# Optimization experiments

Hardware: AMD Instinct MI355X
Metric: run time of the kernel (lower is better)

## Reference

```python
import jax, jax.numpy as jnp
import numpy as np

B, T, D, H = 2, 2048, 1024, 16
NEG = -65504.0


def setup_inputs() -> dict:
    key = jax.random.key(0)
    ks = jax.random.split(key, 12)
    std = float(np.sqrt(2.0 / (D + D)))  # xavier_normal for square weights
    inp = {
        'q': jax.random.normal(ks[0], (B, T, D), jnp.float32),
        'k': jax.random.normal(ks[1], (B, T, D), jnp.float32),
        'v': jax.random.normal(ks[2], (B, T, D), jnp.float32),
        'mask': jax.random.randint(ks[3], (B, T), 0, 2, jnp.int32),
        # weights stored as (in, out) so y = x @ W + b
        'Wq': jax.random.normal(ks[4], (D, D), jnp.float32) * std,
        'bq': jnp.zeros((D,), jnp.float32),
        'Wk': jax.random.normal(ks[5], (D, D), jnp.float32) * std,
        'bk': jnp.zeros((D,), jnp.float32),
        'Wv': jax.random.normal(ks[6], (D, D), jnp.float32) * std,
        'bv': jnp.zeros((D,), jnp.float32),
        'Wo': jax.random.normal(ks[7], (D, D), jnp.float32) * std,
        'bo': jnp.zeros((D,), jnp.float32),
    }
    return inp


def reference(q, k, v, mask, Wq, bq, Wk, bk, Wv, bv, Wo, bo):
    b, t, _ = q.shape
    dim_a = Wq.shape[1]
    dh = dim_a // H
    # projections, then split into heads: (b, t, H, dh)
    qh = (q @ Wq + bq).reshape(b, t, H, dh)
    kh = (k @ Wk + bk).reshape(b, t, H, dh)
    vh = (v @ Wv + bv).reshape(b, t, H, dh)
    # NOTE: module scales by 1/sqrt(dim_a) with the FULL dim_a, not per-head
    a = jnp.einsum('bthd,bshd->bhts', qh, kh) / jnp.sqrt(jnp.float32(dim_a))
    # 2D mask broadcasts over query positions: (b, 1, 1, t_keys)
    a = jnp.where(mask[:, None, None, :] == 0, NEG, a)
    a = jax.nn.softmax(a, axis=-1)  # dropout_prob=0 (eval mode)
    o = jnp.einsum('bhts,bshd->bthd', a, vh).reshape(b, t, dim_a)
    return o @ Wo + bo
```

## Files before the change

### kernel.cpp

```cpp
#include <hip/hip_runtime.h>
#include <hip/hip_bf16.h>
#include <math.h>

#define B_ 2
#define T_ 2048
#define D_ 1024
#define H_ 16
#define QSCALE (0.03125f * 1.44269504088896f)

typedef _Float16 f16;
using f16x4 = __attribute__((ext_vector_type(4))) _Float16;
using f16x8 = __attribute__((ext_vector_type(8))) _Float16;
using f32x4 = __attribute__((ext_vector_type(4))) float;

__device__ __forceinline__ void gl16(const void* g, void* l) {
  __builtin_amdgcn_global_load_lds(
      (__attribute__((address_space(1))) void*)g,
      (__attribute__((address_space(3))) void*)l, 16, 0, 0);
}

__device__ __forceinline__ unsigned lds_a32(const void* p) {
  return (unsigned)(size_t)(__attribute__((address_space(3))) const char*)p;
}

__global__ __launch_bounds__(256) void prep0(
    const int* __restrict__ mask, int* __restrict__ inv, int* __restrict__ nk) {
  __shared__ int cnt[256];
  const int b = blockIdx.x;
  const int tid = threadIdx.x;
  int loc[8];
  int c = 0;
#pragma unroll
  for (int i = 0; i < 8; ++i) {
    loc[i] = mask[b * T_ + tid * 8 + i];
    c += loc[i];
  }
  cnt[tid] = c;
  __syncthreads();
  for (int off = 1; off < 256; off <<= 1) {
    int vsh = (tid >= off) ? cnt[tid - off] : 0;
    __syncthreads();
    cnt[tid] += vsh;
    __syncthreads();
  }
  int pos = cnt[tid] - c;
#pragma unroll
  for (int i = 0; i < 8; ++i) {
    const int t = tid * 8 + i;
    inv[b * T_ + t] = loc[i] ? pos : -1;
    pos += loc[i];
  }
  if (tid == 255) nk[b] = cnt[255];
}

__global__ __launch_bounds__(256) void prep1(
    const float* __restrict__ q, const float* __restrict__ k,
    const float* __restrict__ v, const int* __restrict__ inv,
    const float* __restrict__ Wq, const float* __restrict__ Wk,
    const float* __restrict__ Wv, const float* __restrict__ Wo,
    const float* __restrict__ bq, const float* __restrict__ bk,
    const float* __restrict__ bv, const float* __restrict__ bo,
    f16* __restrict__ xqkv, f16* __restrict__ Wt, float* __restrict__ bias) {
  __shared__ float sh[64][65];
  const int bid = blockIdx.x;
  const int tid = threadIdx.x;

  if (bid < 6144) {
    const int z = bid / 2048;
    const float* src = (z == 0) ? q : (z == 1) ? k : v;
    const size_t i = ((size_t)(bid % 2048) * 256 + tid) * 8;
    float4 a = *(const float4*)(src + i);
    float4 b4 = *(const float4*)(src + i + 4);
    f16x8 o;
    o[0] = (f16)a.x;  o[1] = (f16)a.y;  o[2] = (f16)a.z;  o[3] = (f16)a.w;
    o[4] = (f16)b4.x; o[5] = (f16)b4.y; o[6] = (f16)b4.z; o[7] = (f16)b4.w;
    if (z == 0) {
      *(f16x8*)(xqkv + i) = o;
    } else {
      const int tl = (int)(i >> 10);
      const int bb = tl >> 11, t = tl & 2047;
      const int j = inv[bb * T_ + t];
      if (j >= 0)
        *(f16x8*)(xqkv + (size_t)z * 4194304 +
                  (((size_t)(bb * T_ + j)) << 10) + (i & 1023)) = o;
    }
  } else if (bid < 7168) {
    const int id = bid - 6144;
    const int z = id >> 8;
    const int k0 = ((id >> 4) & 15) * 64, n0 = (id & 15) * 64;
    const float* W = (z == 0) ? Wq : (z == 1) ? Wk : (z == 2) ? Wv : Wo;
    const int r = tid >> 2, c0 = (tid & 3) * 16;
#pragma unroll
    for (int i = 0; i < 4; ++i)
      *(float4*)&sh[r][c0 + 4 * i] =
          *(const float4*)&W[(size_t)(k0 + r) * 1024 + n0 + c0 + 4 * i];
    __syncthreads();
    f16 tmp[16];
#pragma unroll
    for (int i = 0; i < 16; ++i) tmp[i] = (f16)sh[c0 + i][r];
    f16* dst = Wt + (size_t)z * 1048576 + (size_t)(n0 + r) * 1024 + k0 + c0;
    *(f16x8*)dst = *(f16x8*)&tmp[0];
    *(f16x8*)(dst + 8) = *(f16x8*)&tmp[8];
  } else {
    const int i = (bid - 7168) * 256 + tid;
    const int z = i >> 10;
    const float* s = (z == 0) ? bq : (z == 1) ? bk : (z == 2) ? bv : bo;
    bias[i] = s[i & 1023];
  }
}

template <typename OT, bool CMP>
__global__ __launch_bounds__(256, 4) void gemm_r4(
    const f16* __restrict__ Xb, const f16* __restrict__ Wtb,
    const float* __restrict__ biasb, void* __restrict__ C0,
    void* __restrict__ C1, void* __restrict__ C2,
    const int* __restrict__ nkd, float qscale) {
  __shared__ __align__(16) char lds[65536];
  const int z = blockIdx.z;
  const int m0 = blockIdx.y * 128, n0 = blockIdx.x * 128;

  if (CMP && z) {
    const int nb = nkd[m0 >> 11];
    const int lim = ((nb + 63) >> 6) << 6;
    if ((m0 & 2047) >= lim) return;
  }

  const f16* X  = Xb  + (size_t)z * (4096 * 1024);
  const f16* Wt = Wtb + (size_t)z * (1024 * 1024);
  const float* bias = biasb + (size_t)z * 1024;
  OT* C = (OT*)((z == 0) ? C0 : (z == 1) ? C1 : C2);
  const float scl = (z == 0) ? qscale : 1.f;

  const int tid = threadIdx.x;
  const int wave = tid >> 6, lane = tid & 63;
  const int quad = lane >> 4, l16 = lane & 15;
  const int wm = wave & 1, wn = wave >> 1;

  const int r0 = tid >> 2;
  const int ssw = (tid & 3) ^ ((r0 >> 1) & 3);
  const f16* ap0 = X  + (size_t)(m0 + r0) * 1024 + ssw * 8;
  const f16* ap1 = ap0 + (size_t)64 * 1024;
  const f16* bp0 = Wt + (size_t)(n0 + r0) * 1024 + ssw * 8;
  const f16* bp1 = bp0 + (size_t)64 * 1024;
  char* al = lds + tid * 16;
  char* bl = lds + 8192 + tid * 16;

  const int sw16 = 16 * (quad ^ ((l16 >> 1) & 3));
  const unsigned a32 = lds_a32(lds + (64 * wm + l16) * 64 + sw16);
  const unsigned b32 = lds_a32(lds + 8192 + (64 * wn + l16) * 64 + sw16);

  f32x4 acc[4][4] = {};

#define R4_ISSUE(tt, sl) do {                                               \
    gl16(ap0 + (tt) * 32, al + (sl) * 16384);                               \
    gl16(ap1 + (tt) * 32, al + (sl) * 16384 + 4096);                        \
    gl16(bp0 + (tt) * 32, bl + (sl) * 16384);                               \
    gl16(bp1 + (tt) * 32, bl + (sl) * 16384 + 4096);                        \
    __builtin_amdgcn_sched_barrier(0);                                      \
  } while (0)

#define R4_WAIT(n) do {                                                     \
    asm volatile("s_waitcnt vmcnt(" #n ")");                                \
    __builtin_amdgcn_sched_barrier(0);                                      \
  } while (0)

#define R4_BAR() do {                                                       \
    __builtin_amdgcn_sched_barrier(0);                                      \
    asm volatile("s_barrier");                                              \
    __builtin_amdgcn_sched_barrier(0);                                      \
  } while (0)

#define R4_STR_(x) #x
#define R4_STR(x) R4_STR_(x)
#define DSR(dst, base, OFF)                                                 \
  asm volatile("ds_read_b128 %0, %1 offset:" R4_STR(OFF)                    \
               : "=v"(dst) : "v"(base))

#define R4_COMPUTE(sl) do {                                                 \
    R4_BAR();                                                               \
    const unsigned aa = a32 + (sl) * 16384;                                 \
    const unsigned bb = b32 + (sl) * 16384;                                 \
    f16x8 af[4], bf[4];                                                     \
    DSR(af[0], aa, 0);    DSR(af[1], aa, 1024);                             \
    DSR(bf[0], bb, 0);    DSR(bf[1], bb, 1024);                             \
    DSR(bf[2], bb, 2048); DSR(bf[3], bb, 3072);                             \
    DSR(af[2], aa, 2048); DSR(af[3], aa, 3072);                             \
    asm volatile("s_waitcnt lgkmcnt(2)");                                   \
    __builtin_amdgcn_sched_barrier(0);                                      \
    __builtin_amdgcn_s_setprio(1);                                          \
    _Pragma("unroll")                                                       \
    for (int mi = 0; mi < 2; ++mi)                                          \
      _Pragma("unroll")                                                     \
      for (int ni = 0; ni < 4; ++ni)                                        \
        acc[mi][ni] = __builtin_amdgcn_mfma_f32_16x16x32_f16(               \
            af[mi], bf[ni], acc[mi][ni], 0, 0, 0);                          \
    asm volatile("s_waitcnt lgkmcnt(0)");                                   \
    __builtin_amdgcn_sched_barrier(0);                                      \
    _Pragma("unroll")                                                       \
    for (int mi = 2; mi < 4; ++mi)                                          \
      _Pragma("unroll")                                                     \
      for (int ni = 0; ni < 4; ++ni)                                        \
        acc[mi][ni] = __builtin_amdgcn_mfma_f32_16x16x32_f16(               \
            af[mi], bf[ni], acc[mi][ni], 0, 0, 0);                          \
    __builtin_amdgcn_s_setprio(0);                                          \
    R4_BAR();                                                               \
  } while (0)

  R4_ISSUE(0, 0); R4_ISSUE(1, 1); R4_ISSUE(2, 2);

  for (int j = 0; j < 7; ++j) {
    const int t4 = j * 4;
    R4_ISSUE(t4 + 3, 3); R4_WAIT(12); R4_COMPUTE(0);
    R4_ISSUE(t4 + 4, 0); R4_WAIT(12); R4_COMPUTE(1);
    R4_ISSUE(t4 + 5, 1); R4_WAIT(12); R4_COMPUTE(2);
    R4_ISSUE(t4 + 6, 2); R4_WAIT(12); R4_COMPUTE(3);
  }
  R4_ISSUE(31, 3); R4_WAIT(12); R4_COMPUTE(0);
  R4_WAIT(8);  R4_COMPUTE(1);
  R4_WAIT(4);  R4_COMPUTE(2);
  R4_WAIT(0);  R4_COMPUTE(3);

#undef R4_ISSUE
#undef R4_WAIT
#undef R4_BAR
#undef DSR
#undef R4_STR
#undef R4_STR_
#undef R4_COMPUTE

  const int cm = m0 + 64 * wm + 4 * quad;
  const int cn = n0 + 64 * wn + l16;
  float bv[4];
#pragma unroll
  for (int ni = 0; ni < 4; ++ni) bv[ni] = bias[cn + 16 * ni];

  if (!CMP || z == 0) {
#pragma unroll
    for (int mi = 0; mi < 4; ++mi)
#pragma unroll
      for (int r = 0; r < 4; ++r) {
        OT* row = C + (size_t)(cm + 16 * mi + r) * 1024;
#pragma unroll
        for (int ni = 0; ni < 4; ++ni)
          row[cn + 16 * ni] = (OT)((acc[mi][ni][r] + bv[ni]) * scl);
      }
  } else {
    const int nb = nkd[m0 >> 11];
#pragma unroll
    for (int mi = 0; mi < 4; ++mi)
#pragma unroll
      for (int r = 0; r < 4; ++r) {
        const int m = cm + 16 * mi + r;
        const bool ok = (m & 2047) < nb;
        OT* row = C + (size_t)m * 1024;
#pragma unroll
        for (int ni = 0; ni < 4; ++ni)
          row[cn + 16 * ni] = ok ? (OT)(acc[mi][ni][r] + bv[ni]) : (OT)0.f;
      }
  }
}

__global__ __launch_bounds__(256) void vtrans(
    const f16* __restrict__ vhc, const int* __restrict__ nk,
    f16* __restrict__ vhT) {
  const int tt = blockIdx.x, bh = blockIdx.y;
  const int b = bh >> 4, h = bh & 15;
  const int n = nk[b];
  const int nkt = (n + 63) >> 6;
  if (tt >= nkt) return;
  __shared__ f16 t[64][72];
  const int tid = threadIdx.x;
  const int r = tid >> 2, cq = 16 * (tid & 3);

  const int j = tt * 64 + r;
  uint4 v0 = {0u, 0u, 0u, 0u}, v1 = {0u, 0u, 0u, 0u};
  if (j < n) {
    const uint4* src = (const uint4*)(vhc + ((size_t)b * T_ + j) * D_ + h * 64 + cq);
    v0 = src[0]; v1 = src[1];
  }
  *(uint4*)&t[r][cq]     = v0;
  *(uint4*)&t[r][cq + 8] = v1;
  __syncthreads();

  f16 tmp[16];
#pragma unroll
  for (int xx = 0; xx < 16; ++xx) {
    int x = (xx + r) & 15;
    tmp[x] = t[cq + x][r];
  }
  f16* dst = vhT + ((size_t)bh * 64 + r) * T_ + tt * 64 + cq;
  *(uint4*)&dst[0] = *(uint4*)&tmp[0];
  *(uint4*)&dst[8] = *(uint4*)&tmp[8];
}

__global__ __launch_bounds__(512) void attn_mfma(
    const f16* __restrict__ qh, const f16* __restrict__ khc,
    const f16* __restrict__ vhT, const int* __restrict__ nkd,
    f16* __restrict__ oat) {
  __shared__ f16 Ks[64][72];
  __shared__ f16 Vt[64][72];
  __shared__ f16 Ps[8][16][72];

  const int qt = blockIdx.x, bh = blockIdx.y;
  const int b = bh >> 4, h = bh & 15;
  const int tid = threadIdx.x;
  const int wave = tid >> 6, lane = tid & 63;
  const int quad = lane >> 4, l16 = lane & 15;
  const int sr = tid >> 3, sq = 8 * (tid & 7);

  const int n = nkd[b];
  const int nkt = (n + 63) >> 6;
  const int npad = (nkt << 6) - n;

  f16x8 qf[2];
  {
    const f16* qp = qh + ((size_t)(b * T_ + qt * 128 + wave * 16 + l16)) * D_ + h * 64 + quad * 8;
    qf[0] = *(const f16x8*)qp;
    qf[1] = *(const f16x8*)(qp + 32);
  }

  float lsum = 0.f;
  f32x4 o[4] = {};

  const f16* kbase = khc + (size_t)b * T_ * D_ + h * 64;
  const f16* vbase = vhT + ((size_t)bh * 64 + sr) * T_;

  uint4 kr, vr;
  auto load_kv = [&](int kt) {
    kr = *(const uint4*)(kbase + (size_t)(kt * 64 + sr) * D_ + sq);
    vr = *(const uint4*)(vbase + kt * 64 + sq);
  };
  if (nkt > 0) load_kv(0);

  for (int kt = 0; kt < nkt; ++kt) {
    *(uint4*)&Ks[sr][sq] = kr;
    *(uint4*)&Vt[sr][sq] = vr;
    __syncthreads();
    if (kt + 1 < nkt) load_kv(kt + 1);

#pragma unroll
    for (int tn = 0; tn < 4; ++tn) {
      f16x8 kf0 = *(const f16x8*)&Ks[16 * tn + l16][quad * 8];
      f16x8 kf1 = *(const f16x8*)&Ks[16 * tn + l16][32 + quad * 8];
      f32x4 s = {0.f, 0.f, 0.f, 0.f};
      s = __builtin_amdgcn_mfma_f32_16x16x32_f16(kf0, qf[0], s, 0, 0, 0);
      s = __builtin_amdgcn_mfma_f32_16x16x32_f16(kf1, qf[1], s, 0, 0, 0);
      float p0 = exp2f(s[0]), p1 = exp2f(s[1]);
      float p2 = exp2f(s[2]), p3 = exp2f(s[3]);
      lsum += (p0 + p1) + (p2 + p3);
      f16x4 pk;
      pk[0] = (f16)p0; pk[1] = (f16)p1; pk[2] = (f16)p2; pk[3] = (f16)p3;
      *(f16x4*)&Ps[wave][l16][16 * tn + 4 * quad] = pk;
    }

    f16x8 pf0 = *(const f16x8*)&Ps[wave][l16][quad * 8];
    f16x8 pf1 = *(const f16x8*)&Ps[wave][l16][32 + quad * 8];
#pragma unroll
    for (int t = 0; t < 4; ++t) {
      f16x8 vf0 = *(const f16x8*)&Vt[16 * t + l16][quad * 8];
      f16x8 vf1 = *(const f16x8*)&Vt[16 * t + l16][32 + quad * 8];
      o[t] = __builtin_amdgcn_mfma_f32_16x16x32_f16(pf0, vf0, o[t], 0, 0, 0);
      o[t] = __builtin_amdgcn_mfma_f32_16x16x32_f16(pf1, vf1, o[t], 0, 0, 0);
    }
    __syncthreads();
  }

  {
    float ls = lsum;
    ls += __shfl_xor(ls, 16);
    ls += __shfl_xor(ls, 32);
    ls -= (float)npad;
    const size_t orow = (size_t)(b * T_ + qt * 128 + wave * 16 + 4 * quad);
#pragma unroll
    for (int r = 0; r < 4; ++r) {
      const float iv = 1.f / __shfl(ls, 4 * quad + r);
#pragma unroll
      for (int t = 0; t < 4; ++t)
        oat[(orow + r) * D_ + h * 64 + 16 * t + l16] = (f16)(o[t][r] * iv);
    }
  }
}

extern "C" void kernel_launch(void* const* d_in, const int* in_sizes, int n_in,
                              void* d_out, int out_size, void* d_ws, size_t ws_size,
                              hipStream_t stream) {
  const float* q  = (const float*)d_in[0];
  const float* k  = (const float*)d_in[1];
  const float* v  = (const float*)d_in[2];
  const int* mask = (const int*)d_in[3];
  const float* Wq = (const float*)d_in[4];
  const float* bq = (const float*)d_in[5];
  const float* Wk = (const float*)d_in[6];
  const float* bk = (const float*)d_in[7];
  const float* Wv = (const float*)d_in[8];
  const float* bv = (const float*)d_in[9];
  const float* Wo = (const float*)d_in[10];
  const float* bo = (const float*)d_in[11];
  float* out = (float*)d_out;

  char* ws = (char*)d_ws;
  f16* xqkv  = (f16*)(ws);
  f16* Wt    = (f16*)(ws + 25165824);
  f16* qh    = (f16*)(ws + 33554432);
  f16* vhc   = (f16*)(ws + 41943040);
  f16* khc   = (f16*)(ws + 50331648);
  float* bsw = (float*)(ws + 58720256);
  int* inv   = (int*)(ws + 58736640);
  int* nk    = (int*)(ws + 58753024);
  f16* vhT   = (f16*)(ws);
  f16* oat   = (f16*)(ws + 8388608);

  dim3 blk(256);

  prep0<<<dim3(2), blk, 0, stream>>>(mask, inv, nk);

  prep1<<<dim3(7184), blk, 0, stream>>>(q, k, v, inv, Wq, Wk, Wv, Wo,
                                        bq, bk, bv, bo, xqkv, Wt, bsw);

  gemm_r4<f16, true><<<dim3(8, 32, 3), blk, 0, stream>>>(
      xqkv, Wt, bsw, qh, khc, vhc, nk, QSCALE);

  vtrans<<<dim3(32, 32), blk, 0, stream>>>(vhc, nk, vhT);

  attn_mfma<<<dim3(16, 32), dim3(512), 0, stream>>>(qh, khc, vhT, nk, oat);

  gemm_r4<float, false><<<dim3(8, 32, 1), blk, 0, stream>>>(
      oat, Wt + 3145728, bsw + 3072, out, nullptr, nullptr, nullptr, 1.f);
}
```

Baseline: 217.0 us.

## Fuse V transpose into QKV GEMM epilogue and narrow output GEMM tiles

The QKV projection GEMM now writes the V projection directly in head-transposed layout (per head, dh x T) with packed f16x4 stores, which removes the separate vtrans kernel and its extra global round trip. The GEMM is templated on the N-tile width, and the output projection uses 128x64 tiles with twice as many blocks, so its 256 blocks on a single z slice fill more of the device. The transposed epilogue writes are strided by T and only 8 bytes wide, which may coalesce less well than the old row stores.

```diff
diff --git a/kernel.cpp b/kernel.cpp
--- a/kernel.cpp
+++ b/kernel.cpp
@@ -109,15 +109,16 @@
   }
 }
 
-template <typename OT, bool CMP>
+template <typename OT, bool CMP, int FN>
 __global__ __launch_bounds__(256, 4) void gemm_r4(
     const f16* __restrict__ Xb, const f16* __restrict__ Wtb,
     const float* __restrict__ biasb, void* __restrict__ C0,
     void* __restrict__ C1, void* __restrict__ C2,
     const int* __restrict__ nkd, float qscale) {
+  static_assert(FN == 2 || FN == 4, "FN must be 2 or 4");
   __shared__ __align__(16) char lds[65536];
   const int z = blockIdx.z;
-  const int m0 = blockIdx.y * 128, n0 = blockIdx.x * 128;
+  const int m0 = blockIdx.y * 128, n0 = blockIdx.x * (32 * FN);
 
   if (CMP && z) {
     const int nb = nkd[m0 >> 11];
@@ -147,20 +148,27 @@
 
   const int sw16 = 16 * (quad ^ ((l16 >> 1) & 3));
   const unsigned a32 = lds_a32(lds + (64 * wm + l16) * 64 + sw16);
-  const unsigned b32 = lds_a32(lds + 8192 + (64 * wn + l16) * 64 + sw16);
-
-  f32x4 acc[4][4] = {};
+  const unsigned b32 = lds_a32(lds + 8192 + (16 * FN * wn + l16) * 64 + sw16);
+
+  f32x4 acc[4][FN] = {};
 
 #define R4_ISSUE(tt, sl) do {                                               \
     gl16(ap0 + (tt) * 32, al + (sl) * 16384);                               \
     gl16(ap1 + (tt) * 32, al + (sl) * 16384 + 4096);                        \
     gl16(bp0 + (tt) * 32, bl + (sl) * 16384);                               \
-    gl16(bp1 + (tt) * 32, bl + (sl) * 16384 + 4096);                        \
+    if constexpr (FN == 4) gl16(bp1 + (tt) * 32, bl + (sl) * 16384 + 4096); \
     __builtin_amdgcn_sched_barrier(0);                                      \
   } while (0)
 
-#define R4_WAIT(n) do {                                                     \
-    asm volatile("s_waitcnt vmcnt(" #n ")");                                \
+#define R4_WAITM() do {                                                     \
+    if constexpr (FN == 4) { asm volatile("s_waitcnt vmcnt(12)"); }         \
+    else                   { asm volatile("s_waitcnt vmcnt(9)");  }         \
+    __builtin_amdgcn_sched_barrier(0);                                      \
+  } while (0)
+
+#define R4_WAITE(n4, n2) do {                                               \
+    if constexpr (FN == 4) { asm volatile("s_waitcnt vmcnt(" #n4 ")"); }    \
+    else                   { asm volatile("s_waitcnt vmcnt(" #n2 ")"); }    \
     __builtin_amdgcn_sched_barrier(0);                                      \
   } while (0)
 
@@ -180,10 +188,10 @@
     R4_BAR();                                                               \
     const unsigned aa = a32 + (sl) * 16384;                                 \
     const unsigned bb = b32 + (sl) * 16384;                                 \
-    f16x8 af[4], bf[4];                                                     \
+    f16x8 af[4], bf[FN];                                                    \
     DSR(af[0], aa, 0);    DSR(af[1], aa, 1024);                             \
     DSR(bf[0], bb, 0);    DSR(bf[1], bb, 1024);                             \
-    DSR(bf[2], bb, 2048); DSR(bf[3], bb, 3072);                             \
+    if constexpr (FN == 4) { DSR(bf[2], bb, 2048); DSR(bf[3], bb, 3072); }  \
     DSR(af[2], aa, 2048); DSR(af[3], aa, 3072);                             \
     asm volatile("s_waitcnt lgkmcnt(2)");                                   \
     __builtin_amdgcn_sched_barrier(0);                                      \
@@ -191,7 +199,7 @@
     _Pragma("unroll")                                                       \
     for (int mi = 0; mi < 2; ++mi)                                          \
       _Pragma("unroll")                                                     \
-      for (int ni = 0; ni < 4; ++ni)                                        \
+      for (int ni = 0; ni < FN; ++ni)                                       \
         acc[mi][ni] = __builtin_amdgcn_mfma_f32_16x16x32_f16(               \
             af[mi], bf[ni], acc[mi][ni], 0, 0, 0);                          \
     asm volatile("s_waitcnt lgkmcnt(0)");                                   \
@@ -199,7 +207,7 @@
     _Pragma("unroll")                                                       \
     for (int mi = 2; mi < 4; ++mi)                                          \
       _Pragma("unroll")                                                     \
-      for (int ni = 0; ni < 4; ++ni)                                        \
+      for (int ni = 0; ni < FN; ++ni)                                       \
         acc[mi][ni] = __builtin_amdgcn_mfma_f32_16x16x32_f16(               \
             af[mi], bf[ni], acc[mi][ni], 0, 0, 0);                          \
     __builtin_amdgcn_s_setprio(0);                                          \
@@ -210,18 +218,19 @@
 
   for (int j = 0; j < 7; ++j) {
     const int t4 = j * 4;
-    R4_ISSUE(t4 + 3, 3); R4_WAIT(12); R4_COMPUTE(0);
-    R4_ISSUE(t4 + 4, 0); R4_WAIT(12); R4_COMPUTE(1);
-    R4_ISSUE(t4 + 5, 1); R4_WAIT(12); R4_COMPUTE(2);
-    R4_ISSUE(t4 + 6, 2); R4_WAIT(12); R4_COMPUTE(3);
-  }
-  R4_ISSUE(31, 3); R4_WAIT(12); R4_COMPUTE(0);
-  R4_WAIT(8);  R4_COMPUTE(1);
-  R4_WAIT(4);  R4_COMPUTE(2);
-  R4_WAIT(0);  R4_COMPUTE(3);
+    R4_ISSUE(t4 + 3, 3); R4_WAITM(); R4_COMPUTE(0);
+    R4_ISSUE(t4 + 4, 0); R4_WAITM(); R4_COMPUTE(1);
+    R4_ISSUE(t4 + 5, 1); R4_WAITM(); R4_COMPUTE(2);
+    R4_ISSUE(t4 + 6, 2); R4_WAITM(); R4_COMPUTE(3);
+  }
+  R4_ISSUE(31, 3); R4_WAITM(); R4_COMPUTE(0);
+  R4_WAITE(8, 6);  R4_COMPUTE(1);
+  R4_WAITE(4, 3);  R4_COMPUTE(2);
+  R4_WAITE(0, 0);  R4_COMPUTE(3);
 
 #undef R4_ISSUE
-#undef R4_WAIT
+#undef R4_WAITM
+#undef R4_WAITE
 #undef R4_BAR
 #undef DSR
 #undef R4_STR
@@ -229,10 +238,10 @@
 #undef R4_COMPUTE
 
   const int cm = m0 + 64 * wm + 4 * quad;
-  const int cn = n0 + 64 * wn + l16;
-  float bv[4];
-#pragma unroll
-  for (int ni = 0; ni < 4; ++ni) bv[ni] = bias[cn + 16 * ni];
+  const int cn = n0 + 16 * FN * wn + l16;
+  float bv[FN];
+#pragma unroll
+  for (int ni = 0; ni < FN; ++ni) bv[ni] = bias[cn + 16 * ni];
 
   if (!CMP || z == 0) {
 #pragma unroll
@@ -241,10 +250,10 @@
       for (int r = 0; r < 4; ++r) {
         OT* row = C + (size_t)(cm + 16 * mi + r) * 1024;
 #pragma unroll
-        for (int ni = 0; ni < 4; ++ni)
+        for (int ni = 0; ni < FN; ++ni)
           row[cn + 16 * ni] = (OT)((acc[mi][ni][r] + bv[ni]) * scl);
       }
-  } else {
+  } else if (z == 1) {
     const int nb = nkd[m0 >> 11];
 #pragma unroll
     for (int mi = 0; mi < 4; ++mi)
@@ -254,43 +263,29 @@
         const bool ok = (m & 2047) < nb;
         OT* row = C + (size_t)m * 1024;
 #pragma unroll
-        for (int ni = 0; ni < 4; ++ni)
+        for (int ni = 0; ni < FN; ++ni)
           row[cn + 16 * ni] = ok ? (OT)(acc[mi][ni][r] + bv[ni]) : (OT)0.f;
       }
-  }
-}
-
-__global__ __launch_bounds__(256) void vtrans(
-    const f16* __restrict__ vhc, const int* __restrict__ nk,
-    f16* __restrict__ vhT) {
-  const int tt = blockIdx.x, bh = blockIdx.y;
-  const int b = bh >> 4, h = bh & 15;
-  const int n = nk[b];
-  const int nkt = (n + 63) >> 6;
-  if (tt >= nkt) return;
-  __shared__ f16 t[64][72];
-  const int tid = threadIdx.x;
-  const int r = tid >> 2, cq = 16 * (tid & 3);
-
-  const int j = tt * 64 + r;
-  uint4 v0 = {0u, 0u, 0u, 0u}, v1 = {0u, 0u, 0u, 0u};
-  if (j < n) {
-    const uint4* src = (const uint4*)(vhc + ((size_t)b * T_ + j) * D_ + h * 64 + cq);
-    v0 = src[0]; v1 = src[1];
-  }
-  *(uint4*)&t[r][cq]     = v0;
-  *(uint4*)&t[r][cq + 8] = v1;
-  __syncthreads();
-
-  f16 tmp[16];
-#pragma unroll
-  for (int xx = 0; xx < 16; ++xx) {
-    int x = (xx + r) & 15;
-    tmp[x] = t[cq + x][r];
-  }
-  f16* dst = vhT + ((size_t)bh * 64 + r) * T_ + tt * 64 + cq;
-  *(uint4*)&dst[0] = *(uint4*)&tmp[0];
-  *(uint4*)&dst[8] = *(uint4*)&tmp[8];
+  } else {
+    const int nb = nkd[m0 >> 11];
+    const int bb = m0 >> 11;
+    const int jb = cm & 2047;
+#pragma unroll
+    for (int mi = 0; mi < 4; ++mi) {
+      const int j0 = jb + 16 * mi;
+#pragma unroll
+      for (int ni = 0; ni < FN; ++ni) {
+        const int c = cn + 16 * ni;
+        f16x4 pk;
+#pragma unroll
+        for (int r = 0; r < 4; ++r)
+          pk[r] = (j0 + r < nb) ? (f16)(acc[mi][ni][r] + bv[ni]) : (f16)0.f;
+        f16* dst = (f16*)C +
+            (((size_t)(bb * 16 + (c >> 6)) * 64 + (c & 63)) << 11) + j0;
+        *(f16x4*)dst = pk;
+      }
+    }
+  }
 }
 
 __global__ __launch_bounds__(512) void attn_mfma(
@@ -402,12 +397,11 @@
   f16* xqkv  = (f16*)(ws);
   f16* Wt    = (f16*)(ws + 25165824);
   f16* qh    = (f16*)(ws + 33554432);
-  f16* vhc   = (f16*)(ws + 41943040);
+  f16* vhT   = (f16*)(ws + 41943040);
   f16* khc   = (f16*)(ws + 50331648);
   float* bsw = (float*)(ws + 58720256);
   int* inv   = (int*)(ws + 58736640);
   int* nk    = (int*)(ws + 58753024);
-  f16* vhT   = (f16*)(ws);
   f16* oat   = (f16*)(ws + 8388608);
 
   dim3 blk(256);
@@ -417,13 +411,11 @@
   prep1<<<dim3(7184), blk, 0, stream>>>(q, k, v, inv, Wq, Wk, Wv, Wo,
                                         bq, bk, bv, bo, xqkv, Wt, bsw);
 
-  gemm_r4<f16, true><<<dim3(8, 32, 3), blk, 0, stream>>>(
-      xqkv, Wt, bsw, qh, khc, vhc, nk, QSCALE);
-
-  vtrans<<<dim3(32, 32), blk, 0, stream>>>(vhc, nk, vhT);
+  gemm_r4<f16, true, 4><<<dim3(8, 32, 3), blk, 0, stream>>>(
+      xqkv, Wt, bsw, qh, khc, vhT, nk, QSCALE);
 
   attn_mfma<<<dim3(16, 32), dim3(512), 0, stream>>>(qh, khc, vhT, nk, oat);
 
-  gemm_r4<float, false><<<dim3(8, 32, 1), blk, 0, stream>>>(
+  gemm_r4<float, false, 2><<<dim3(16, 32, 1), blk, 0, stream>>>(
       oat, Wt + 3145728, bsw + 3072, out, nullptr, nullptr, nullptr, 1.f);
 }
```

Result: faster. 209.5 us (-3.4%).
